# Optimization experiments

Measured on AMD Instinct MI355X. Metric: run time of the kernel, lower is better.

## Reference

```python
import jax, jax.numpy as jnp
import numpy as np

HEADS = 8  # init heads


def setup_inputs() -> dict:
    key = jax.random.key(0)
    k1, k2, k3, k4 = jax.random.split(key, 4)
    B, C, L = 32, 512, 32  # batch, dim, lateral_size
    x = jax.random.normal(k1, (B, C, L, L), dtype=jnp.float32)
    # 1x1 conv with no bias == per-pixel matmul; store as [3*dim, dim]
    qkv_w = jax.random.normal(k2, (3 * C, C), dtype=jnp.float32) * (1.0 / np.sqrt(C))
    h_pos = jax.random.normal(k3, (L, 1, C), dtype=jnp.float32) * 0.02
    w_pos = jax.random.normal(k4, (1, L, C), dtype=jnp.float32) * 0.02
    return {"x": x, "qkv_w": qkv_w, "h_pos": h_pos, "w_pos": w_pos}


def reference(x, qkv_w, h_pos, w_pos):
    B, C, H, W = x.shape
    p = HEADS
    d = C // p
    n = H * W
    # QKV 1x1 conv -> [B, 3C, H, W]
    qkv = jnp.einsum('oc,bchw->bohw', qkv_w, x)
    q, k, v = jnp.split(qkv, 3, axis=1)
    # 'b (p d) h w -> b p (h w) d'
    def to_heads(t):
        return t.reshape(B, p, d, H, W).transpose(0, 1, 3, 4, 2).reshape(B, p, n, d)
    q, k, v = to_heads(q), to_heads(k), to_heads(v)
    # relative pos: [H,1,C] + [1,W,C] -> [H,W,C]; 'h w (p d) -> p (h w) d'
    rp = (h_pos + w_pos).reshape(H, W, p, d).transpose(2, 0, 1, 3).reshape(p, n, d)
    # content-position + content-content scores: [B, p, n, n]
    scores = jnp.einsum('bpnd,pmd->bpnm', q, rp) + jnp.einsum('bpnd,bpmd->bpnm', q, k)
    attn = jax.nn.softmax(scores, axis=-1)
    out = jnp.einsum('bpnm,bpmd->bpnd', attn, v)
    # 'b p (h w) d -> b (p d) h w'
    return out.reshape(B, p, H, W, d).transpose(0, 1, 4, 2, 3).reshape(B, C, H, W)
```

## Files before the change

### kernel.cpp

```cpp
#include <hip/hip_runtime.h>
#include <hip/hip_bf16.h>
#include <hip/hip_fp16.h>

#define HEADS 8
#define BB 32
#define CC 512
#define NN 1024
#define DD 64

typedef _Float16 f16;
typedef __attribute__((ext_vector_type(8))) _Float16 f16x8;
typedef __attribute__((ext_vector_type(4))) _Float16 f16x4;
typedef __attribute__((ext_vector_type(2))) __fp16 hf16x2;
typedef __attribute__((ext_vector_type(4))) float f32x4;

__device__ __forceinline__ void gload16(const f16* g, f16* l) {
    __builtin_amdgcn_global_load_lds(
        (const __attribute__((address_space(1))) void*)g,
        (__attribute__((address_space(3))) void*)l, 16, 0, 0);
}

__device__ __forceinline__ void wavefence() {
    asm volatile("s_waitcnt lgkmcnt(0)" ::: "memory");
}

__global__ __launch_bounds__(256) void wconv(
    const float* __restrict__ W, f16* __restrict__ Wh)
{
    const size_t i = ((size_t)blockIdx.x * 256 + threadIdx.x) * 8;
    float4 a = *(const float4*)(W + i);
    float4 b = *(const float4*)(W + i + 4);
    f16x8 h = {(f16)a.x, (f16)a.y, (f16)a.z, (f16)a.w,
               (f16)b.x, (f16)b.y, (f16)b.z, (f16)b.w};
    *(f16x8*)(Wh + i) = h;
}

__global__ __launch_bounds__(256) void prep_x(
    const float* __restrict__ x, f16* __restrict__ xt)
{
    __shared__ f16 T[64][65];
    const int tid = threadIdx.x;
    const int c0 = blockIdx.x * 64;
    const int m0 = blockIdx.y * 64;
    const int b  = blockIdx.z;
    const float* xb = x + (size_t)b * CC * NN;

    const int m_l = tid & 63, c_l = tid >> 6;
    #pragma unroll
    for (int s = 0; s < 16; ++s) {
        const int cr = s * 4 + c_l;
        T[cr][m_l] = (f16)xb[(size_t)(c0 + cr) * NN + m0 + m_l];
    }
    __syncthreads();
    const int m_r = tid >> 2, cq = (tid & 3) * 16;
    f16 buf[16];
    #pragma unroll
    for (int j = 0; j < 16; ++j) buf[j] = T[cq + j][m_r];
    f16* dst = xt + ((size_t)b * NN + m0 + m_r) * CC + c0 + cq;
    *(f16x8*)dst       = *(f16x8*)&buf[0];
    *(f16x8*)(dst + 8) = *(f16x8*)&buf[8];
}

__global__ __launch_bounds__(256) void qkv_mfma(
    const f16*  __restrict__ xt,
    const f16*  __restrict__ Wh,
    const float* __restrict__ h_pos,
    const float* __restrict__ w_pos,
    f16* __restrict__ Qh, f16* __restrict__ Kh, f16* __restrict__ Vt)
{
    __shared__ f16 SM[2 * 128 * 64];
    f16* Xs = SM;
    f16* Ws = SM + 128 * 64;

    const int tid  = threadIdx.x;
    const int wave = tid >> 6, lane = tid & 63;
    const int ln = lane & 15, quad = lane >> 4;

    const unsigned bid  = blockIdx.x;
    const unsigned xcd  = bid & 7;
    const unsigned slot = bid >> 3;
    const unsigned ot   = slot % 12u;
    const unsigned mt   = xcd * 32u + slot / 12u;
    const int o0  = (int)ot * 128;
    const int mg0 = (int)mt * 128;
    const int mw = (wave & 1) * 64, ow = (wave >> 1) * 64;

    f32x4 acc[4][4];
    #pragma unroll
    for (int ia = 0; ia < 4; ++ia)
        #pragma unroll
        for (int ib = 0; ib < 4; ++ib) acc[ia][ib] = (f32x4){0.f, 0.f, 0.f, 0.f};

    const int sr = wave * 32 + (lane >> 3);
    const int sc = (lane & 7) * 8;
    const f16* xg = xt + (size_t)(mg0 + sr) * CC + sc;
    const f16* wg = Wh + (size_t)(o0  + sr) * CC + sc;
    f16* xl = &Xs[(wave * 32) * 64];
    f16* wl = &Ws[(wave * 32) * 64];

    for (int ct = 0; ct < 8; ++ct) {
        const int c0 = ct * 64;
        __syncthreads();
        #pragma unroll
        for (int i = 0; i < 4; ++i) {
            gload16(xg + (size_t)i * 8 * CC + c0, xl + i * 8 * 64);
            gload16(wg + (size_t)i * 8 * CC + c0, wl + i * 8 * 64);
        }
        __syncthreads();
        #pragma unroll
        for (int ks = 0; ks < 2; ++ks) {
            f16x8 a[4], bf[4];
            #pragma unroll
            for (int f = 0; f < 4; ++f) {
                a[f]  = *(const f16x8*)&Xs[(mw + f * 16 + ln) * 64 + ks * 32 + quad * 8];
                bf[f] = *(const f16x8*)&Ws[(ow + f * 16 + ln) * 64 + ks * 32 + quad * 8];
            }
            #pragma unroll
            for (int ia = 0; ia < 4; ++ia)
                #pragma unroll
                for (int ib = 0; ib < 4; ++ib)
                    acc[ia][ib] = __builtin_amdgcn_mfma_f32_16x16x32_f16(
                        a[ia], bf[ib], acc[ia][ib], 0, 0, 0);
        }
    }

    __syncthreads();
    f16* Ep = SM + wave * 4096;

    const int region = o0 >> 9;
    const int ob = o0 + ow;
    const int p  = (ob >> 6) & 7;
    const int b  = mg0 >> 10;
    const int n0 = (mg0 & 1023) + mw;

    if (region < 2) {
        f16* dst = (region == 0) ? Qh : Kh;
        const size_t hb = (size_t)(b * HEADS + p) * NN * DD;
        #pragma unroll
        for (int ph = 0; ph < 2; ++ph) {
            #pragma unroll
            for (int ibl = 0; ibl < 2; ++ibl) {
                const int ib = ph * 2 + ibl;
                const int d  = ib * 16 + ln;
                const int dl = ibl * 16 + ln;
                #pragma unroll
                for (int ia = 0; ia < 4; ++ia) {
                    #pragma unroll
                    for (int r = 0; r < 4; ++r) {
                        const int nl = ia * 16 + quad * 4 + r;
                        float v = acc[ia][ib][r];
                        if (region == 0) {
                            v *= 1.44269504f;
                        } else {
                            const int n = n0 + nl;
                            const int c = p * DD + d;
                            v += h_pos[(n >> 5) * CC + c] + w_pos[(n & 31) * CC + c];
                        }
                        Ep[nl * 34 + dl] = (f16)v;
                    }
                }
            }
            wavefence();
            #pragma unroll
            for (int j = 0; j < 4; ++j) {
                const int nl = (lane >> 2) + 16 * j;
                const int dc = (lane & 3) * 8;
                f16x8 row = *(const f16x8*)&Ep[nl * 34 + dc];
                *(f16x8*)(dst + hb + (size_t)(n0 + nl) * DD + ph * 32 + dc) = row;
            }
            wavefence();
        }
    } else {
        const size_t vb = (size_t)(b * HEADS + p) * DD * NN;
        #pragma unroll
        for (int ph = 0; ph < 2; ++ph) {
            #pragma unroll
            for (int ibl = 0; ibl < 2; ++ibl) {
                const int ib = ph * 2 + ibl;
                const int dl = ibl * 16 + ln;
                #pragma unroll
                for (int ia = 0; ia < 4; ++ia) {
                    const int nl = ia * 16 + quad * 4;
                    f16x4 pk = {(f16)acc[ia][ib][0], (f16)acc[ia][ib][1],
                                (f16)acc[ia][ib][2], (f16)acc[ia][ib][3]};
                    *(f16x4*)&Ep[dl * 68 + nl] = pk;
                }
            }
            wavefence();
            #pragma unroll
            for (int j = 0; j < 4; ++j) {
                const int dl = (lane >> 3) + 8 * j;
                const int nc = (lane & 7) * 8;
                f16x8 row = *(const f16x8*)&Ep[dl * 68 + nc];
                *(f16x8*)(Vt + vb + (size_t)(ph * 32 + dl) * NN + n0 + nc) = row;
            }
            wavefence();
        }
    }
}

#define KST 72

__global__ __launch_bounds__(256) void attn_kernel(
    const f16* __restrict__ Qh, const f16* __restrict__ Kh,
    const f16* __restrict__ Vt, float* __restrict__ out)
{
    __shared__ f16 KS [64 * KST];
    __shared__ f16 VtS[64 * KST];
    __shared__ f16 PS [4][16 * KST];

    const int tid  = threadIdx.x;
    const int wave = tid >> 6;
    const int lane = tid & 63;
    const int ln   = lane & 15;
    const int quad = lane >> 4;

    const unsigned bid  = blockIdx.x;
    const unsigned xcd  = bid & 7;
    const unsigned slot = bid >> 3;
    const int qt = (int)(slot & 15u);
    const unsigned g = xcd * 32u + (slot >> 4);
    const int b = (int)(g >> 3);
    const int p = (int)(g & 7u);
    const size_t hb = (size_t)(b * HEADS + p) * NN * DD;

    const int qrow = qt * 64 + wave * 16 + ln;
    f16x8 qf[2];
    #pragma unroll
    for (int ks = 0; ks < 2; ++ks)
        qf[ks] = *(const f16x8*)(Qh + hb + (size_t)qrow * DD + ks * 32 + quad * 8);

    f32x4 o[4];
    #pragma unroll
    for (int dt = 0; dt < 4; ++dt) o[dt] = (f32x4){0.f, 0.f, 0.f, 0.f};
    float lrun = 0.f;
    float mrun = -__builtin_inff();
    const float THR = 11.5416f;

    const int sr = tid >> 2, sc = (tid & 3) * 16;

    f16x8 kreg0, kreg1, vreg0, vreg1;
    {
        const size_t gk = hb + (size_t)sr * DD + sc;
        kreg0 = *(const f16x8*)(Kh + gk);
        kreg1 = *(const f16x8*)(Kh + gk + 8);
        const size_t gv = hb + (size_t)sr * NN + sc;
        vreg0 = *(const f16x8*)(Vt + gv);
        vreg1 = *(const f16x8*)(Vt + gv + 8);
    }

    f16* Pw = &PS[wave][0];

    for (int kt = 0; kt < 16; ++kt) {
        __syncthreads();
        *(f16x8*)&KS [sr * KST + sc]     = kreg0;
        *(f16x8*)&KS [sr * KST + sc + 8] = kreg1;
        *(f16x8*)&VtS[sr * KST + sc]     = vreg0;
        *(f16x8*)&VtS[sr * KST + sc + 8] = vreg1;
        if (kt < 15) {
            const size_t gk = hb + (size_t)((kt + 1) * 64 + sr) * DD + sc;
            kreg0 = *(const f16x8*)(Kh + gk);
            kreg1 = *(const f16x8*)(Kh + gk + 8);
            const size_t gv = hb + (size_t)sr * NN + (kt + 1) * 64 + sc;
            vreg0 = *(const f16x8*)(Vt + gv);
            vreg1 = *(const f16x8*)(Vt + gv + 8);
        }
        __syncthreads();

        f32x4 s[4];
        #pragma unroll
        for (int nt = 0; nt < 4; ++nt) s[nt] = (f32x4){0.f, 0.f, 0.f, 0.f};
        #pragma unroll
        for (int ks = 0; ks < 2; ++ks) {
            #pragma unroll
            for (int nt = 0; nt < 4; ++nt) {
                f16x8 bk = *(const f16x8*)&KS[(nt * 16 + ln) * KST + ks * 32 + quad * 8];
                s[nt] = __builtin_amdgcn_mfma_f32_16x16x32_f16(bk, qf[ks], s[nt], 0, 0, 0);
            }
        }

        float mx = s[0][0];
        #pragma unroll
        for (int nt = 0; nt < 4; ++nt)
            #pragma unroll
            for (int r = 0; r < 4; ++r) mx = fmaxf(mx, s[nt][r]);
        mx = fmaxf(mx, __shfl_xor(mx, 16));
        mx = fmaxf(mx, __shfl_xor(mx, 32));

        if (__any(mx > mrun + THR)) {
            const float mnew = fmaxf(mrun, mx);
            const float alpha = __builtin_amdgcn_exp2f(mrun - mnew);
            mrun = mnew;
            lrun *= alpha;
            #pragma unroll
            for (int dt = 0; dt < 4; ++dt) {
                o[dt][0] *= alpha; o[dt][1] *= alpha;
                o[dt][2] *= alpha; o[dt][3] *= alpha;
            }
        }

        float lsum = 0.f;
        #pragma unroll
        for (int nt = 0; nt < 4; ++nt) {
            const float p0 = __builtin_amdgcn_exp2f(s[nt][0] - mrun);
            const float p1 = __builtin_amdgcn_exp2f(s[nt][1] - mrun);
            const float p2 = __builtin_amdgcn_exp2f(s[nt][2] - mrun);
            const float p3 = __builtin_amdgcn_exp2f(s[nt][3] - mrun);
            lsum += (p0 + p1) + (p2 + p3);
            hf16x2 lo = __builtin_amdgcn_cvt_pkrtz(p0, p1);
            hf16x2 hi = __builtin_amdgcn_cvt_pkrtz(p2, p3);
            f16x4 pk = {(f16)lo.x, (f16)lo.y, (f16)hi.x, (f16)hi.y};
            *(f16x4*)&Pw[ln * KST + nt * 16 + quad * 4] = pk;
        }
        lsum += __shfl_xor(lsum, 16);
        lsum += __shfl_xor(lsum, 32);
        lrun += lsum;

        asm volatile("s_waitcnt lgkmcnt(0)" ::: "memory");

        #pragma unroll
        for (int ks = 0; ks < 2; ++ks) {
            f16x8 pa = *(const f16x8*)&Pw[ln * KST + ks * 32 + quad * 8];
            #pragma unroll
            for (int dt = 0; dt < 4; ++dt) {
                f16x8 vb = *(const f16x8*)&VtS[(dt * 16 + ln) * KST + ks * 32 + quad * 8];
                o[dt] = __builtin_amdgcn_mfma_f32_16x16x32_f16(vb, pa, o[dt], 0, 0, 0);
            }
        }
    }

    const float inv = 1.0f / lrun;
    const int nq = qt * 64 + wave * 16 + ln;
    #pragma unroll
    for (int dt = 0; dt < 4; ++dt) {
        const int c = p * DD + dt * 16 + quad * 4;
        #pragma unroll
        for (int r = 0; r < 4; ++r)
            out[((size_t)b * CC + c + r) * NN + nq] = o[dt][r] * inv;
    }
}

extern "C" void kernel_launch(void* const* d_in, const int* in_sizes, int n_in,
                              void* d_out, int out_size, void* d_ws, size_t ws_size,
                              hipStream_t stream) {
    const float* x     = (const float*)d_in[0];
    const float* qkv_w = (const float*)d_in[1];
    const float* h_pos = (const float*)d_in[2];
    const float* w_pos = (const float*)d_in[3];
    float* out = (float*)d_out;

    const size_t PT = (size_t)BB * HEADS * NN * DD;
    f16* xt = (f16*)d_ws;
    f16* Qh = xt + PT;
    f16* Kh = Qh + PT;
    f16* Vt = Kh + PT;
    f16* Wh = Vt + PT;

    wconv<<<dim3(3 * CC * CC / (256 * 8)), 256, 0, stream>>>(qkv_w, Wh);
    prep_x<<<dim3(CC / 64, NN / 64, BB), 256, 0, stream>>>(x, xt);
    qkv_mfma<<<dim3(3072), 256, 0, stream>>>(xt, Wh, h_pos, w_pos, Qh, Kh, Vt);
    attn_kernel<<<dim3(4096), 256, 0, stream>>>(Qh, Kh, Vt, out);
}
```

Measured before the change: 368.7 us.

## Process two 16-row query tiles per wave in attention kernel

Each wave now handles 32 query rows (two MFMA tiles), so each block covers 128 queries and the grid halves to 2048 blocks. Every K and V tile staged in LDS is reused across twice as many queries, which halves the global K/V traffic and LDS staging per query. The LDS row stride also changes from 72 to 76 halves, likely to alter bank-conflict patterns. In exchange it raises register and LDS use per wave and reduces the number of blocks available for latency hiding.

Measured after the change: 396.1 us. +7.4%, slower.

```diff
diff --git a/kernel.cpp b/kernel.cpp
--- a/kernel.cpp
+++ b/kernel.cpp
@@ -199,7 +199,7 @@
     }
 }
 
-#define KST 72
+#define KST 76
 
 __global__ __launch_bounds__(256) void attn_kernel(
     const f16* __restrict__ Qh, const f16* __restrict__ Kh,
@@ -207,7 +207,7 @@
 {
     __shared__ f16 KS [64 * KST];
     __shared__ f16 VtS[64 * KST];
-    __shared__ f16 PS [4][16 * KST];
+    __shared__ f16 PS [4][32 * KST];
 
     const int tid  = threadIdx.x;
     const int wave = tid >> 6;
@@ -218,23 +218,28 @@
     const unsigned bid  = blockIdx.x;
     const unsigned xcd  = bid & 7;
     const unsigned slot = bid >> 3;
-    const int qt = (int)(slot & 15u);
-    const unsigned g = xcd * 32u + (slot >> 4);
+    const int qt = (int)(slot & 7u);
+    const unsigned g = xcd * 32u + (slot >> 3);
     const int b = (int)(g >> 3);
     const int p = (int)(g & 7u);
     const size_t hb = (size_t)(b * HEADS + p) * NN * DD;
 
-    const int qrow = qt * 64 + wave * 16 + ln;
-    f16x8 qf[2];
-    #pragma unroll
-    for (int ks = 0; ks < 2; ++ks)
-        qf[ks] = *(const f16x8*)(Qh + hb + (size_t)qrow * DD + ks * 32 + quad * 8);
-
-    f32x4 o[4];
-    #pragma unroll
-    for (int dt = 0; dt < 4; ++dt) o[dt] = (f32x4){0.f, 0.f, 0.f, 0.f};
-    float lrun = 0.f;
-    float mrun = -__builtin_inff();
+    const int qbase = qt * 128 + wave * 32;
+    f16x8 qf[2][2];
+    #pragma unroll
+    for (int qa = 0; qa < 2; ++qa)
+        #pragma unroll
+        for (int ks = 0; ks < 2; ++ks)
+            qf[qa][ks] = *(const f16x8*)(
+                Qh + hb + (size_t)(qbase + qa * 16 + ln) * DD + ks * 32 + quad * 8);
+
+    f32x4 o[2][4];
+    #pragma unroll
+    for (int qa = 0; qa < 2; ++qa)
+        #pragma unroll
+        for (int dt = 0; dt < 4; ++dt) o[qa][dt] = (f32x4){0.f, 0.f, 0.f, 0.f};
+    float lrun[2] = {0.f, 0.f};
+    float mrun[2] = {-__builtin_inff(), -__builtin_inff()};
     const float THR = 11.5416f;
 
     const int sr = tid >> 2, sc = (tid & 3) * 16;
@@ -267,76 +272,95 @@
         }
         __syncthreads();
 
-        f32x4 s[4];
-        #pragma unroll
-        for (int nt = 0; nt < 4; ++nt) s[nt] = (f32x4){0.f, 0.f, 0.f, 0.f};
+        f32x4 s[2][4];
+        #pragma unroll
+        for (int qa = 0; qa < 2; ++qa)
+            #pragma unroll
+            for (int nt = 0; nt < 4; ++nt) s[qa][nt] = (f32x4){0.f, 0.f, 0.f, 0.f};
         #pragma unroll
         for (int ks = 0; ks < 2; ++ks) {
             #pragma unroll
             for (int nt = 0; nt < 4; ++nt) {
                 f16x8 bk = *(const f16x8*)&KS[(nt * 16 + ln) * KST + ks * 32 + quad * 8];
-                s[nt] = __builtin_amdgcn_mfma_f32_16x16x32_f16(bk, qf[ks], s[nt], 0, 0, 0);
-            }
-        }
-
-        float mx = s[0][0];
-        #pragma unroll
-        for (int nt = 0; nt < 4; ++nt)
-            #pragma unroll
-            for (int r = 0; r < 4; ++r) mx = fmaxf(mx, s[nt][r]);
-        mx = fmaxf(mx, __shfl_xor(mx, 16));
-        mx = fmaxf(mx, __shfl_xor(mx, 32));
-
-        if (__any(mx > mrun + THR)) {
-            const float mnew = fmaxf(mrun, mx);
-            const float alpha = __builtin_amdgcn_exp2f(mrun - mnew);
-            mrun = mnew;
-            lrun *= alpha;
-            #pragma unroll
-            for (int dt = 0; dt < 4; ++dt) {
-                o[dt][0] *= alpha; o[dt][1] *= alpha;
-                o[dt][2] *= alpha; o[dt][3] *= alpha;
-            }
-        }
-
-        float lsum = 0.f;
-        #pragma unroll
-        for (int nt = 0; nt < 4; ++nt) {
-            const float p0 = __builtin_amdgcn_exp2f(s[nt][0] - mrun);
-            const float p1 = __builtin_amdgcn_exp2f(s[nt][1] - mrun);
-            const float p2 = __builtin_amdgcn_exp2f(s[nt][2] - mrun);
-            const float p3 = __builtin_amdgcn_exp2f(s[nt][3] - mrun);
-            lsum += (p0 + p1) + (p2 + p3);
-            hf16x2 lo = __builtin_amdgcn_cvt_pkrtz(p0, p1);
-            hf16x2 hi = __builtin_amdgcn_cvt_pkrtz(p2, p3);
-            f16x4 pk = {(f16)lo.x, (f16)lo.y, (f16)hi.x, (f16)hi.y};
-            *(f16x4*)&Pw[ln * KST + nt * 16 + quad * 4] = pk;
-        }
-        lsum += __shfl_xor(lsum, 16);
-        lsum += __shfl_xor(lsum, 32);
-        lrun += lsum;
+                s[0][nt] = __builtin_amdgcn_mfma_f32_16x16x32_f16(bk, qf[0][ks], s[0][nt], 0, 0, 0);
+                s[1][nt] = __builtin_amdgcn_mfma_f32_16x16x32_f16(bk, qf[1][ks], s[1][nt], 0, 0, 0);
+            }
+        }
+
+        float mx[2];
+        #pragma unroll
+        for (int qa = 0; qa < 2; ++qa) {
+            float m0 = s[qa][0][0];
+            #pragma unroll
+            for (int nt = 0; nt < 4; ++nt)
+                #pragma unroll
+                for (int r = 0; r < 4; ++r) m0 = fmaxf(m0, s[qa][nt][r]);
+            m0 = fmaxf(m0, __shfl_xor(m0, 16));
+            m0 = fmaxf(m0, __shfl_xor(m0, 32));
+            mx[qa] = m0;
+        }
+
+        if (__any(mx[0] > mrun[0] + THR || mx[1] > mrun[1] + THR)) {
+            #pragma unroll
+            for (int qa = 0; qa < 2; ++qa) {
+                const float mnew = fmaxf(mrun[qa], mx[qa]);
+                const float alpha = __builtin_amdgcn_exp2f(mrun[qa] - mnew);
+                mrun[qa] = mnew;
+                lrun[qa] *= alpha;
+                #pragma unroll
+                for (int dt = 0; dt < 4; ++dt) {
+                    o[qa][dt][0] *= alpha; o[qa][dt][1] *= alpha;
+                    o[qa][dt][2] *= alpha; o[qa][dt][3] *= alpha;
+                }
+            }
+        }
+
+        #pragma unroll
+        for (int qa = 0; qa < 2; ++qa) {
+            float lsum = 0.f;
+            #pragma unroll
+            for (int nt = 0; nt < 4; ++nt) {
+                const float p0 = __builtin_amdgcn_exp2f(s[qa][nt][0] - mrun[qa]);
+                const float p1 = __builtin_amdgcn_exp2f(s[qa][nt][1] - mrun[qa]);
+                const float p2 = __builtin_amdgcn_exp2f(s[qa][nt][2] - mrun[qa]);
+                const float p3 = __builtin_amdgcn_exp2f(s[qa][nt][3] - mrun[qa]);
+                lsum += (p0 + p1) + (p2 + p3);
+                hf16x2 lo = __builtin_amdgcn_cvt_pkrtz(p0, p1);
+                hf16x2 hi = __builtin_amdgcn_cvt_pkrtz(p2, p3);
+                f16x4 pk = {(f16)lo.x, (f16)lo.y, (f16)hi.x, (f16)hi.y};
+                *(f16x4*)&Pw[(qa * 16 + ln) * KST + nt * 16 + quad * 4] = pk;
+            }
+            lsum += __shfl_xor(lsum, 16);
+            lsum += __shfl_xor(lsum, 32);
+            lrun[qa] += lsum;
+        }
 
         asm volatile("s_waitcnt lgkmcnt(0)" ::: "memory");
 
         #pragma unroll
         for (int ks = 0; ks < 2; ++ks) {
-            f16x8 pa = *(const f16x8*)&Pw[ln * KST + ks * 32 + quad * 8];
+            f16x8 pa0 = *(const f16x8*)&Pw[(ln)      * KST + ks * 32 + quad * 8];
+            f16x8 pa1 = *(const f16x8*)&Pw[(16 + ln) * KST + ks * 32 + quad * 8];
             #pragma unroll
             for (int dt = 0; dt < 4; ++dt) {
                 f16x8 vb = *(const f16x8*)&VtS[(dt * 16 + ln) * KST + ks * 32 + quad * 8];
-                o[dt] = __builtin_amdgcn_mfma_f32_16x16x32_f16(vb, pa, o[dt], 0, 0, 0);
-            }
-        }
-    }
-
-    const float inv = 1.0f / lrun;
-    const int nq = qt * 64 + wave * 16 + ln;
-    #pragma unroll
-    for (int dt = 0; dt < 4; ++dt) {
-        const int c = p * DD + dt * 16 + quad * 4;
-        #pragma unroll
-        for (int r = 0; r < 4; ++r)
-            out[((size_t)b * CC + c + r) * NN + nq] = o[dt][r] * inv;
+                o[0][dt] = __builtin_amdgcn_mfma_f32_16x16x32_f16(vb, pa0, o[0][dt], 0, 0, 0);
+                o[1][dt] = __builtin_amdgcn_mfma_f32_16x16x32_f16(vb, pa1, o[1][dt], 0, 0, 0);
+            }
+        }
+    }
+
+    #pragma unroll
+    for (int qa = 0; qa < 2; ++qa) {
+        const float inv = 1.0f / lrun[qa];
+        const int nq = qbase + qa * 16 + ln;
+        #pragma unroll
+        for (int dt = 0; dt < 4; ++dt) {
+            const int c = p * DD + dt * 16 + quad * 4;
+            #pragma unroll
+            for (int r = 0; r < 4; ++r)
+                out[((size_t)b * CC + c + r) * NN + nq] = o[qa][dt][r] * inv;
+        }
     }
 }
 
@@ -359,5 +383,5 @@
     wconv<<<dim3(3 * CC * CC / (256 * 8)), 256, 0, stream>>>(qkv_w, Wh);
     prep_x<<<dim3(CC / 64, NN / 64, BB), 256, 0, stream>>>(x, xt);
     qkv_mfma<<<dim3(3072), 256, 0, stream>>>(xt, Wh, h_pos, w_pos, Qh, Kh, Vt);
-    attn_kernel<<<dim3(4096), 256, 0, stream>>>(Qh, Kh, Vt, out);
-}
+    attn_kernel<<<dim3(2048), 256, 0, stream>>>(Qh, Kh, Vt, out);
+}
```

## Switch attention to 32x32x16 MFMA with register-resident P via permlane32 swap

Applied to the files above, without the earlier changes.

Rewrites the attention inner loop to use 32x32x16 MFMA tiles, with each wave handling 32 query rows in a 128-thread block. The P matrix is repacked in registers with permlane32_swap and no longer goes through an LDS round-trip. Row max and sum reductions also use permlane swaps instead of shuffles. The aim is to cut LDS traffic and waits, at the cost of higher register pressure and fewer threads to share each K/V tile load.

Result: faster. 357.5 us (-3.1%).

```diff
diff --git a/kernel.cpp b/kernel.cpp
--- a/kernel.cpp
+++ b/kernel.cpp
@@ -13,6 +13,8 @@
 typedef __attribute__((ext_vector_type(4))) _Float16 f16x4;
 typedef __attribute__((ext_vector_type(2))) __fp16 hf16x2;
 typedef __attribute__((ext_vector_type(4))) float f32x4;
+typedef __attribute__((ext_vector_type(16))) float f32x16;
+typedef __attribute__((ext_vector_type(4))) unsigned u32x4;
 
 __device__ __forceinline__ void gload16(const f16* g, f16* l) {
     __builtin_amdgcn_global_load_lds(
@@ -22,6 +24,22 @@
 
 __device__ __forceinline__ void wavefence() {
     asm volatile("s_waitcnt lgkmcnt(0)" ::: "memory");
+}
+
+__device__ __forceinline__ void pl32swap(unsigned &a, unsigned &b) {
+    auto r = __builtin_amdgcn_permlane32_swap(a, b, false, false);
+    a = r[0]; b = r[1];
+}
+
+__device__ __forceinline__ float xhalf_max(float x) {
+    unsigned a = __float_as_uint(x), b = a;
+    pl32swap(a, b);
+    return fmaxf(__uint_as_float(a), __uint_as_float(b));
+}
+__device__ __forceinline__ float xhalf_sum(float x) {
+    unsigned a = __float_as_uint(x), b = a;
+    pl32swap(a, b);
+    return __uint_as_float(a) + __uint_as_float(b);
 }
 
 __global__ __launch_bounds__(256) void wconv(
@@ -199,21 +217,20 @@
     }
 }
 
-#define KST 72
-
-__global__ __launch_bounds__(256) void attn_kernel(
+#define KST 76
+
+__global__ __launch_bounds__(128) void attn_kernel(
     const f16* __restrict__ Qh, const f16* __restrict__ Kh,
     const f16* __restrict__ Vt, float* __restrict__ out)
 {
     __shared__ f16 KS [64 * KST];
     __shared__ f16 VtS[64 * KST];
-    __shared__ f16 PS [4][16 * KST];
 
     const int tid  = threadIdx.x;
     const int wave = tid >> 6;
     const int lane = tid & 63;
-    const int ln   = lane & 15;
-    const int quad = lane >> 4;
+    const int l31  = lane & 31;
+    const int h    = lane >> 5;
 
     const unsigned bid  = blockIdx.x;
     const unsigned xcd  = bid & 7;
@@ -224,68 +241,58 @@
     const int p = (int)(g & 7u);
     const size_t hb = (size_t)(b * HEADS + p) * NN * DD;
 
-    const int qrow = qt * 64 + wave * 16 + ln;
-    f16x8 qf[2];
-    #pragma unroll
-    for (int ks = 0; ks < 2; ++ks)
-        qf[ks] = *(const f16x8*)(Qh + hb + (size_t)qrow * DD + ks * 32 + quad * 8);
-
-    f32x4 o[4];
-    #pragma unroll
-    for (int dt = 0; dt < 4; ++dt) o[dt] = (f32x4){0.f, 0.f, 0.f, 0.f};
+    const int qbase = qt * 64 + wave * 32;
+    f16x8 qf[4];
+    #pragma unroll
+    for (int s = 0; s < 4; ++s)
+        qf[s] = *(const f16x8*)(Qh + hb + (size_t)(qbase + l31) * DD + s * 16 + h * 8);
+
+    f32x16 oA = {0.f,0.f,0.f,0.f,0.f,0.f,0.f,0.f,0.f,0.f,0.f,0.f,0.f,0.f,0.f,0.f};
+    f32x16 oB = oA;
     float lrun = 0.f;
     float mrun = -__builtin_inff();
     const float THR = 11.5416f;
 
-    const int sr = tid >> 2, sc = (tid & 3) * 16;
-
-    f16x8 kreg0, kreg1, vreg0, vreg1;
-    {
-        const size_t gk = hb + (size_t)sr * DD + sc;
-        kreg0 = *(const f16x8*)(Kh + gk);
-        kreg1 = *(const f16x8*)(Kh + gk + 8);
-        const size_t gv = hb + (size_t)sr * NN + sc;
-        vreg0 = *(const f16x8*)(Vt + gv);
-        vreg1 = *(const f16x8*)(Vt + gv + 8);
-    }
-
-    f16* Pw = &PS[wave][0];
+    const int tr = tid >> 1, tc = (tid & 1) * 32;
+    f16x8 kr[4], vr[4];
+    #pragma unroll
+    for (int k = 0; k < 4; ++k) {
+        kr[k] = *(const f16x8*)(Kh + hb + (size_t)tr * DD + tc + k * 8);
+        vr[k] = *(const f16x8*)(Vt + hb + (size_t)tr * NN + tc + k * 8);
+    }
 
     for (int kt = 0; kt < 16; ++kt) {
         __syncthreads();
-        *(f16x8*)&KS [sr * KST + sc]     = kreg0;
-        *(f16x8*)&KS [sr * KST + sc + 8] = kreg1;
-        *(f16x8*)&VtS[sr * KST + sc]     = vreg0;
-        *(f16x8*)&VtS[sr * KST + sc + 8] = vreg1;
+        #pragma unroll
+        for (int k = 0; k < 4; ++k) {
+            *(f16x8*)&KS [tr * KST + tc + k * 8] = kr[k];
+            *(f16x8*)&VtS[tr * KST + tc + k * 8] = vr[k];
+        }
         if (kt < 15) {
-            const size_t gk = hb + (size_t)((kt + 1) * 64 + sr) * DD + sc;
-            kreg0 = *(const f16x8*)(Kh + gk);
-            kreg1 = *(const f16x8*)(Kh + gk + 8);
-            const size_t gv = hb + (size_t)sr * NN + (kt + 1) * 64 + sc;
-            vreg0 = *(const f16x8*)(Vt + gv);
-            vreg1 = *(const f16x8*)(Vt + gv + 8);
+            #pragma unroll
+            for (int k = 0; k < 4; ++k) {
+                kr[k] = *(const f16x8*)(Kh + hb + (size_t)((kt + 1) * 64 + tr) * DD + tc + k * 8);
+                vr[k] = *(const f16x8*)(Vt + hb + (size_t)tr * NN + (kt + 1) * 64 + tc + k * 8);
+            }
         }
         __syncthreads();
 
-        f32x4 s[4];
-        #pragma unroll
-        for (int nt = 0; nt < 4; ++nt) s[nt] = (f32x4){0.f, 0.f, 0.f, 0.f};
-        #pragma unroll
-        for (int ks = 0; ks < 2; ++ks) {
-            #pragma unroll
-            for (int nt = 0; nt < 4; ++nt) {
-                f16x8 bk = *(const f16x8*)&KS[(nt * 16 + ln) * KST + ks * 32 + quad * 8];
-                s[nt] = __builtin_amdgcn_mfma_f32_16x16x32_f16(bk, qf[ks], s[nt], 0, 0, 0);
-            }
-        }
-
-        float mx = s[0][0];
-        #pragma unroll
-        for (int nt = 0; nt < 4; ++nt)
-            #pragma unroll
-            for (int r = 0; r < 4; ++r) mx = fmaxf(mx, s[nt][r]);
-        mx = fmaxf(mx, __shfl_xor(mx, 16));
-        mx = fmaxf(mx, __shfl_xor(mx, 32));
+        f32x16 sA = {0.f,0.f,0.f,0.f,0.f,0.f,0.f,0.f,0.f,0.f,0.f,0.f,0.f,0.f,0.f,0.f};
+        f32x16 sB = sA;
+        #pragma unroll
+        for (int s = 0; s < 4; ++s) {
+            f16x8 a0 = *(const f16x8*)&KS[(l31)      * KST + s * 16 + h * 8];
+            f16x8 a1 = *(const f16x8*)&KS[(32 + l31) * KST + s * 16 + h * 8];
+            sA = __builtin_amdgcn_mfma_f32_32x32x16_f16(a0, qf[s], sA, 0, 0, 0);
+            sB = __builtin_amdgcn_mfma_f32_32x32x16_f16(a1, qf[s], sB, 0, 0, 0);
+        }
+
+        float mx = sA[0];
+        #pragma unroll
+        for (int i = 1; i < 16; ++i) mx = fmaxf(mx, sA[i]);
+        #pragma unroll
+        for (int i = 0; i < 16; ++i) mx = fmaxf(mx, sB[i]);
+        mx = xhalf_max(mx);
 
         if (__any(mx > mrun + THR)) {
             const float mnew = fmaxf(mrun, mx);
@@ -293,50 +300,47 @@
             mrun = mnew;
             lrun *= alpha;
             #pragma unroll
-            for (int dt = 0; dt < 4; ++dt) {
-                o[dt][0] *= alpha; o[dt][1] *= alpha;
-                o[dt][2] *= alpha; o[dt][3] *= alpha;
-            }
+            for (int i = 0; i < 16; ++i) { oA[i] *= alpha; oB[i] *= alpha; }
         }
 
         float lsum = 0.f;
         #pragma unroll
-        for (int nt = 0; nt < 4; ++nt) {
-            const float p0 = __builtin_amdgcn_exp2f(s[nt][0] - mrun);
-            const float p1 = __builtin_amdgcn_exp2f(s[nt][1] - mrun);
-            const float p2 = __builtin_amdgcn_exp2f(s[nt][2] - mrun);
-            const float p3 = __builtin_amdgcn_exp2f(s[nt][3] - mrun);
-            lsum += (p0 + p1) + (p2 + p3);
-            hf16x2 lo = __builtin_amdgcn_cvt_pkrtz(p0, p1);
-            hf16x2 hi = __builtin_amdgcn_cvt_pkrtz(p2, p3);
-            f16x4 pk = {(f16)lo.x, (f16)lo.y, (f16)hi.x, (f16)hi.y};
-            *(f16x4*)&Pw[ln * KST + nt * 16 + quad * 4] = pk;
-        }
-        lsum += __shfl_xor(lsum, 16);
-        lsum += __shfl_xor(lsum, 32);
-        lrun += lsum;
-
-        asm volatile("s_waitcnt lgkmcnt(0)" ::: "memory");
-
-        #pragma unroll
-        for (int ks = 0; ks < 2; ++ks) {
-            f16x8 pa = *(const f16x8*)&Pw[ln * KST + ks * 32 + quad * 8];
-            #pragma unroll
-            for (int dt = 0; dt < 4; ++dt) {
-                f16x8 vb = *(const f16x8*)&VtS[(dt * 16 + ln) * KST + ks * 32 + quad * 8];
-                o[dt] = __builtin_amdgcn_mfma_f32_16x16x32_f16(vb, pa, o[dt], 0, 0, 0);
-            }
-        }
+        for (int s = 0; s < 4; ++s) {
+            const f32x16& sk = (s < 2) ? sA : sB;
+            const int base = (s & 1) * 8;
+            const float e0 = __builtin_amdgcn_exp2f(sk[base + 0] - mrun);
+            const float e1 = __builtin_amdgcn_exp2f(sk[base + 1] - mrun);
+            const float e2 = __builtin_amdgcn_exp2f(sk[base + 2] - mrun);
+            const float e3 = __builtin_amdgcn_exp2f(sk[base + 3] - mrun);
+            const float e4 = __builtin_amdgcn_exp2f(sk[base + 4] - mrun);
+            const float e5 = __builtin_amdgcn_exp2f(sk[base + 5] - mrun);
+            const float e6 = __builtin_amdgcn_exp2f(sk[base + 6] - mrun);
+            const float e7 = __builtin_amdgcn_exp2f(sk[base + 7] - mrun);
+            lsum += ((e0 + e1) + (e2 + e3)) + ((e4 + e5) + (e6 + e7));
+            unsigned d00 = __builtin_bit_cast(unsigned, __builtin_amdgcn_cvt_pkrtz(e0, e1));
+            unsigned d01 = __builtin_bit_cast(unsigned, __builtin_amdgcn_cvt_pkrtz(e2, e3));
+            unsigned d10 = __builtin_bit_cast(unsigned, __builtin_amdgcn_cvt_pkrtz(e4, e5));
+            unsigned d11 = __builtin_bit_cast(unsigned, __builtin_amdgcn_cvt_pkrtz(e6, e7));
+            pl32swap(d00, d10);
+            pl32swap(d01, d11);
+            u32x4 pu = {d00, d01, d10, d11};
+            f16x8 pb = __builtin_bit_cast(f16x8, pu);
+            f16x8 v0 = *(const f16x8*)&VtS[(l31)      * KST + s * 16 + h * 8];
+            f16x8 v1 = *(const f16x8*)&VtS[(32 + l31) * KST + s * 16 + h * 8];
+            oA = __builtin_amdgcn_mfma_f32_32x32x16_f16(v0, pb, oA, 0, 0, 0);
+            oB = __builtin_amdgcn_mfma_f32_32x32x16_f16(v1, pb, oB, 0, 0, 0);
+        }
+        lrun += xhalf_sum(lsum);
     }
 
     const float inv = 1.0f / lrun;
-    const int nq = qt * 64 + wave * 16 + ln;
-    #pragma unroll
-    for (int dt = 0; dt < 4; ++dt) {
-        const int c = p * DD + dt * 16 + quad * 4;
-        #pragma unroll
-        for (int r = 0; r < 4; ++r)
-            out[((size_t)b * CC + c + r) * NN + nq] = o[dt][r] * inv;
+    const int nq = qbase + l31;
+    float* ob = out + ((size_t)b * CC + p * DD) * NN + nq;
+    #pragma unroll
+    for (int reg = 0; reg < 16; ++reg) {
+        const int dr = (reg & 3) + 8 * (reg >> 2) + 4 * h;
+        ob[(size_t)dr * NN]        = oA[reg] * inv;
+        ob[(size_t)(32 + dr) * NN] = oB[reg] * inv;
     }
 }
 
@@ -359,5 +363,5 @@
     wconv<<<dim3(3 * CC * CC / (256 * 8)), 256, 0, stream>>>(qkv_w, Wh);
     prep_x<<<dim3(CC / 64, NN / 64, BB), 256, 0, stream>>>(x, xt);
     qkv_mfma<<<dim3(3072), 256, 0, stream>>>(xt, Wh, h_pos, w_pos, Qh, Kh, Vt);
-    attn_kernel<<<dim3(4096), 256, 0, stream>>>(Qh, Kh, Vt, out);
-}
+    attn_kernel<<<dim3(4096), 128, 0, stream>>>(Qh, Kh, Vt, out);
+}
```
